# Optimization experiments

Hardware: AMD Instinct MI355X
Metric: run time of the kernel (lower is better)

## Reference

```python
import jax, jax.numpy as jnp
import numpy as np

TOKENS, D_IN = 8192, 1024
E, D_OUT = 8, 1024
H = 2 * D_OUT  # Expert hidden = 2 * num_outputs


def setup_inputs() -> dict:
    key = jax.random.key(0)
    ks = jax.random.split(key, 4)
    s_in = 1.0 / np.sqrt(D_IN)
    s_h = 1.0 / np.sqrt(H)
    return {
        "x": jax.random.normal(ks[0], (TOKENS, D_IN), dtype=jnp.float32),
        "W1": jax.random.normal(ks[1], (E, D_IN, H), dtype=jnp.float32) * s_in,
        "b1": jnp.zeros((E, H), dtype=jnp.float32),
        "W2": jax.random.normal(ks[2], (E, H, D_OUT), dtype=jnp.float32) * s_h,
        "b2": jnp.zeros((E, D_OUT), dtype=jnp.float32),
        "Wg": jax.random.normal(ks[3], (D_IN, E), dtype=jnp.float32) * s_in,
        "bg": jnp.zeros((E,), dtype=jnp.float32),
    }


def reference(x, W1, b1, W2, b2, Wg, bg):
    # Gating: softmax over experts. gates: [N, E]
    gates = jax.nn.softmax(x @ Wg + bg, axis=-1)
    # All experts run densely: batched GEMM over expert axis.
    h = jax.nn.relu(jnp.einsum('nd,edh->neh', x, W1) + b1)       # [N, E, H]
    expert_out = jnp.einsum('neh,ehf->nef', h, W2) + b2          # [N, E, D_OUT]
    # Gate-weighted sum over experts (fused stack*gate->sum).
    return jnp.einsum('nef,ne->nf', expert_out, gates)            # [N, D_OUT]
```

## Files before the change

### kernel.cpp

```cpp
#include <hip/hip_runtime.h>
#include <stdint.h>

#define TOKENS 8192
#define D_IN   1024
#define NEXP   8
#define D_OUT  1024
#define HDIM   2048
#define KBIG   (NEXP * HDIM)

typedef __bf16 bf16x8 __attribute__((ext_vector_type(8)));
typedef __bf16 bf16x4 __attribute__((ext_vector_type(4)));
typedef float  f32x4  __attribute__((ext_vector_type(4)));

__device__ __forceinline__ void gload16(const void* g, void* l) {
  __builtin_amdgcn_global_load_lds(
      (const __attribute__((address_space(1))) void*)g,
      (__attribute__((address_space(3))) void*)l,
      16, 0, 0);
}

__global__ void gate_kernel(const float* __restrict__ x,
                            const float* __restrict__ Wg,
                            const float* __restrict__ bg,
                            float* __restrict__ gates) {
  const int lane = threadIdx.x & 63;
  const int n = blockIdx.x * 4 + (threadIdx.x >> 6);
  float acc[NEXP];
#pragma unroll
  for (int e = 0; e < NEXP; ++e) acc[e] = 0.f;
  const float* xr = x + (size_t)n * D_IN;
  for (int d = lane; d < D_IN; d += 64) {
    float xv = xr[d];
    const float* wr = Wg + d * NEXP;
#pragma unroll
    for (int e = 0; e < NEXP; ++e) acc[e] += xv * wr[e];
  }
#pragma unroll
  for (int e = 0; e < NEXP; ++e) {
    float v = acc[e];
#pragma unroll
    for (int off = 32; off > 0; off >>= 1) v += __shfl_down(v, off);
    acc[e] = v;
  }
  if (lane == 0) {
    float mx = -1e30f;
#pragma unroll
    for (int e = 0; e < NEXP; ++e) { acc[e] += bg[e]; mx = fmaxf(mx, acc[e]); }
    float s = 0.f;
#pragma unroll
    for (int e = 0; e < NEXP; ++e) { acc[e] = expf(acc[e] - mx); s += acc[e]; }
    float inv = 1.f / s;
#pragma unroll
    for (int e = 0; e < NEXP; ++e) gates[n * NEXP + e] = acc[e] * inv;
  }
}

__global__ void cvt_x_kernel(const float* __restrict__ x, __bf16* __restrict__ xb) {
  const int stride = gridDim.x * blockDim.x;
  const int total4 = TOKENS * D_IN / 4;
  for (int i = blockIdx.x * blockDim.x + threadIdx.x; i < total4; i += stride) {
    float4 v = ((const float4*)x)[i];
    bf16x4 o;
    o[0] = (__bf16)v.x; o[1] = (__bf16)v.y; o[2] = (__bf16)v.z; o[3] = (__bf16)v.w;
    ((bf16x4*)xb)[i] = o;
  }
}

__global__ void transpose_cvt_kernel(const float* __restrict__ W,
                                     __bf16* __restrict__ Wt,
                                     int K, int N, int ldo, size_t ebase) {
  __shared__ float tile[32][33];
  const int e = blockIdx.z;
  const float* Win = W + (size_t)e * K * N;
  __bf16* Wout = Wt + (size_t)e * ebase;
  const int n0 = blockIdx.x * 32;
  const int k0 = blockIdx.y * 32;
  const int tx = threadIdx.x & 31;
  const int ty = threadIdx.x >> 5;
#pragma unroll
  for (int r = ty; r < 32; r += 8)
    tile[r][tx] = Win[(size_t)(k0 + r) * N + n0 + tx];
  __syncthreads();
#pragma unroll
  for (int r = ty; r < 32; r += 8)
    Wout[(size_t)(n0 + r) * ldo + k0 + tx] = (__bf16)tile[tx][r];
}

#define BMR 256
#define BNR 128
#define RSLOT ((BMR + BNR) * 64)

template <int EPI>
__global__ __launch_bounds__(512, 1)
void gemm_ring3(const __bf16* __restrict__ A,
                const __bf16* __restrict__ Bbase, size_t Bstride_e,
                const float* __restrict__ biasbase, int bias_stride_e,
                const float* __restrict__ gates,
                const float* __restrict__ b2,
                int e0, int scale_gate, int first,
                __bf16* __restrict__ Hout, float* __restrict__ Fout,
                int M, int N, int K, int ldo, int ocol_stride_e) {
  __shared__ alignas(16) __bf16 lds[3 * RSLOT];

  const int tid  = threadIdx.x;
  const int lane = tid & 63;
  const int wave = tid >> 6;
  const int wr   = wave >> 1;
  const int wc   = wave & 1;
  const int lrow = lane & 15;
  const int khi  = lane >> 4;
  const int e    = e0 + blockIdx.z;

  const __bf16* Bp   = Bbase + (size_t)e * Bstride_e;
  const float*  bias = biasbase + (size_t)e * bias_stride_e;
  const int     ocol0 = e * ocol_stride_e;

  const int Gx   = gridDim.x;
  const int nwg  = Gx * gridDim.y;
  const int orig = blockIdx.y * Gx + blockIdx.x;
  const int wgid = (orig & 7) * (nwg >> 3) + (orig >> 3);
  const int bn0  = (wgid % Gx) * BNR;
  const int bm0  = (wgid / Gx) * BMR;

  const __bf16* gsrc[6];
#pragma unroll
  for (int i = 0; i < 6; ++i) {
    int o    = i * 8192 + tid * 16;
    bool isA = (o < BMR * 128);
    int oo   = isA ? o : (o - BMR * 128);
    int row  = oo >> 7;
    int scb  = (oo & 127) ^ ((row & 7) << 4);
    gsrc[i] = (isA ? A + (size_t)(bm0 + row) * K
                   : Bp + (size_t)(bn0 + row) * K) + (scb >> 1);
  }

  f32x4 acc[4][4];
#pragma unroll
  for (int m = 0; m < 4; ++m)
#pragma unroll
    for (int n = 0; n < 4; ++n) acc[m][n] = f32x4{0.f, 0.f, 0.f, 0.f};

  const int arow0 = wr * 64 + lrow;
  const int brow0 = wc * 64 + lrow;
  const int sx    = (lrow & 7) << 3;

  auto stage2 = [&](int kt, int s, int p) {
    gload16(gsrc[2 * p]     + (size_t)kt * 64, lds + s * RSLOT + (2 * p) * 4096 + wave * 512);
    gload16(gsrc[2 * p + 1] + (size_t)kt * 64, lds + s * RSLOT + (2 * p + 1) * 4096 + wave * 512);
  };

  const int nk = K >> 6;
  stage2(0, 0, 0); stage2(0, 0, 1); stage2(0, 0, 2);
  if (nk > 1) { stage2(1, 1, 0); stage2(1, 1, 1); stage2(1, 1, 2); }

  int s = 0, s2 = 2;
  for (int t = 0; t < nk; ++t) {
    if (t + 1 < nk) asm volatile("s_waitcnt vmcnt(6)" ::: "memory");
    else            asm volatile("s_waitcnt vmcnt(0)" ::: "memory");
    asm volatile("s_barrier" ::: "memory");

    const __bf16* As = lds + s * RSLOT;
    const __bf16* Bs = As + BMR * 64;
    const bool pf = (t + 2 < nk);

    bf16x8 af[4][2], bfv[4][2];
    auto rdA = [&](int m, int kk) {
      af[m][kk] = *(const bf16x8*)&As[(arow0 + m * 16) * 64 + ((kk * 32 + khi * 8) ^ sx)];
    };
    auto rdB = [&](int n, int kk) {
      bfv[n][kk] = *(const bf16x8*)&Bs[(brow0 + n * 16) * 64 + ((kk * 32 + khi * 8) ^ sx)];
    };
    auto mma = [&](int ms, int ns) {
#pragma unroll
      for (int kk = 0; kk < 2; ++kk)
#pragma unroll
        for (int mi = 0; mi < 2; ++mi)
#pragma unroll
          for (int ni = 0; ni < 2; ++ni)
            acc[ms + mi][ns + ni] = __builtin_amdgcn_mfma_f32_16x16x32_bf16(
                af[ms + mi][kk], bfv[ns + ni][kk], acc[ms + mi][ns + ni], 0, 0, 0);
    };

    rdA(0, 0); rdA(0, 1); rdA(1, 0); rdA(1, 1);
    rdB(0, 0); rdB(0, 1); rdB(1, 0); rdB(1, 1);
    if (pf) stage2(t + 2, s2, 0);
    __builtin_amdgcn_sched_barrier(0);
    __builtin_amdgcn_s_setprio(1); mma(0, 0); __builtin_amdgcn_s_setprio(0);
    __builtin_amdgcn_sched_barrier(0);
    rdB(2, 0); rdB(2, 1); rdB(3, 0); rdB(3, 1);
    if (pf) stage2(t + 2, s2, 1);
    __builtin_amdgcn_sched_barrier(0);
    __builtin_amdgcn_s_setprio(1); mma(0, 2); __builtin_amdgcn_s_setprio(0);
    __builtin_amdgcn_sched_barrier(0);
    rdA(2, 0); rdA(2, 1); rdA(3, 0); rdA(3, 1);
    if (pf) stage2(t + 2, s2, 2);
    __builtin_amdgcn_sched_barrier(0);
    __builtin_amdgcn_s_setprio(1); mma(2, 0); __builtin_amdgcn_s_setprio(0);
    __builtin_amdgcn_sched_barrier(0);
    __builtin_amdgcn_s_setprio(1); mma(2, 2); __builtin_amdgcn_s_setprio(0);

    s  = (s == 2) ? 0 : s + 1;
    s2 = (s2 == 2) ? 0 : s2 + 1;
  }

#pragma unroll
  for (int m = 0; m < 4; ++m) {
    const int grow0 = bm0 + wr * 64 + m * 16 + khi * 4;
    if constexpr (EPI == 0) {
      float g[4];
      if (scale_gate) {
#pragma unroll
        for (int r = 0; r < 4; ++r) g[r] = gates[(size_t)(grow0 + r) * NEXP + e];
      } else {
#pragma unroll
        for (int r = 0; r < 4; ++r) g[r] = 1.f;
      }
#pragma unroll
      for (int n = 0; n < 4; ++n) {
        const int lc = bn0 + wc * 64 + n * 16 + lrow;
        const float bv = bias[lc];
        f32x4 a = acc[m][n];
#pragma unroll
        for (int r = 0; r < 4; ++r) {
          float v = a[r] + bv;
          v = v > 0.f ? v : 0.f;
          Hout[(size_t)(grow0 + r) * ldo + ocol0 + lc] = (__bf16)(v * g[r]);
        }
      }
    } else if constexpr (EPI == 1) {
      float g[4];
#pragma unroll
      for (int r = 0; r < 4; ++r) g[r] = gates[(size_t)(grow0 + r) * NEXP + e];
#pragma unroll
      for (int n = 0; n < 4; ++n) {
        const int lc = bn0 + wc * 64 + n * 16 + lrow;
        const float bv = bias[lc];
        f32x4 a = acc[m][n];
#pragma unroll
        for (int r = 0; r < 4; ++r) {
          float v = (a[r] + bv) * g[r];
          float* o = Fout + (size_t)(grow0 + r) * ldo + lc;
          if (first) *o = v;
          else       *o += v;
        }
      }
    } else {
      float gv[4][NEXP];
#pragma unroll
      for (int r = 0; r < 4; ++r)
#pragma unroll
        for (int j = 0; j < NEXP; ++j)
          gv[r][j] = gates[(size_t)(grow0 + r) * NEXP + j];
#pragma unroll
      for (int n = 0; n < 4; ++n) {
        const int lc = bn0 + wc * 64 + n * 16 + lrow;
        float b2v[NEXP];
#pragma unroll
        for (int j = 0; j < NEXP; ++j) b2v[j] = b2[j * N + lc];
        f32x4 a = acc[m][n];
#pragma unroll
        for (int r = 0; r < 4; ++r) {
          float bias2 = 0.f;
#pragma unroll
          for (int j = 0; j < NEXP; ++j) bias2 += gv[r][j] * b2v[j];
          Fout[(size_t)(grow0 + r) * ldo + lc] = a[r] + bias2;
        }
      }
    }
  }
}

extern "C" void kernel_launch(void* const* d_in, const int* in_sizes, int n_in,
                              void* d_out, int out_size, void* d_ws, size_t ws_size,
                              hipStream_t stream) {
  const float* x  = (const float*)d_in[0];
  const float* W1 = (const float*)d_in[1];
  const float* b1 = (const float*)d_in[2];
  const float* W2 = (const float*)d_in[3];
  const float* b2 = (const float*)d_in[4];
  const float* Wg = (const float*)d_in[5];
  const float* bg = (const float*)d_in[6];
  float* out = (float*)d_out;

  char* w = (char*)d_ws;
  float* gates = (float*)w;   w += (size_t)TOKENS * NEXP * 4;
  __bf16* xb   = (__bf16*)w;  w += (size_t)TOKENS * D_IN * 2;
  __bf16* w1t  = (__bf16*)w;  w += (size_t)NEXP * HDIM * D_IN * 2;
  __bf16* w2t  = (__bf16*)w;  w += (size_t)NEXP * D_OUT * HDIM * 2;
  __bf16* hbuf = (__bf16*)w;

  const size_t need_fused =
      (size_t)TOKENS * NEXP * 4 + (size_t)TOKENS * D_IN * 2 +
      (size_t)NEXP * HDIM * D_IN * 2 + (size_t)NEXP * D_OUT * HDIM * 2 +
      (size_t)TOKENS * KBIG * 2;
  const bool fused = (ws_size >= need_fused);

  gate_kernel<<<TOKENS / 4, 256, 0, stream>>>(x, Wg, bg, gates);
  cvt_x_kernel<<<2048, 256, 0, stream>>>(x, xb);
  transpose_cvt_kernel<<<dim3(HDIM / 32, D_IN / 32, NEXP), 256, 0, stream>>>(
      W1, w1t, D_IN, HDIM, D_IN, (size_t)HDIM * D_IN);

  if (fused) {
    transpose_cvt_kernel<<<dim3(D_OUT / 32, HDIM / 32, NEXP), 256, 0, stream>>>(
        W2, w2t, HDIM, D_OUT, KBIG, (size_t)HDIM);
    gemm_ring3<0><<<dim3(HDIM / BNR, TOKENS / BMR, NEXP), 512, 0, stream>>>(
        xb, w1t, (size_t)HDIM * D_IN, b1, HDIM, gates, nullptr,
        0, 1, 0, hbuf, nullptr, TOKENS, HDIM, D_IN, KBIG, HDIM);
    gemm_ring3<2><<<dim3(D_OUT / BNR, TOKENS / BMR, 1), 512, 0, stream>>>(
        hbuf, w2t, 0, b2, 0, gates, b2,
        0, 0, 0, nullptr, out, TOKENS, D_OUT, KBIG, D_OUT, 0);
  } else {
    transpose_cvt_kernel<<<dim3(D_OUT / 32, HDIM / 32, NEXP), 256, 0, stream>>>(
        W2, w2t, HDIM, D_OUT, HDIM, (size_t)D_OUT * HDIM);
    for (int e = 0; e < NEXP; ++e) {
      gemm_ring3<0><<<dim3(HDIM / BNR, TOKENS / BMR, 1), 512, 0, stream>>>(
          xb, w1t, (size_t)HDIM * D_IN, b1, HDIM, gates, nullptr,
          e, 0, 0, hbuf, nullptr, TOKENS, HDIM, D_IN, HDIM, 0);
      gemm_ring3<1><<<dim3(D_OUT / BNR, TOKENS / BMR, 1), 512, 0, stream>>>(
          hbuf, w2t, (size_t)D_OUT * HDIM, b2, D_OUT, gates, nullptr,
          e, 0, (e == 0) ? 1 : 0, nullptr, out, TOKENS, D_OUT, HDIM, D_OUT, 0);
    }
  }
}
```

Measured before the change: 760.7 us.

## Replace 3-stage GEMM ring with templated 4-stage K=32 pipeline and larger tiles

Rewrites the bf16 MFMA GEMM as a templated kernel with a 4-slot LDS ring over K-steps of 32 and a prefetch distance of three. Block and warp tiles become template parameters: the first GEMM uses 256x256 tiles over a 2x4 wave grid, and the second keeps 256x128. The XOR swizzle on LDS is dropped, and the MFMA work is split into sub-steps with barriers between them. The aim is more load/compute overlap and more reuse per tile in the first GEMM. In exchange it adds more barriers per K-step, and the unswizzled LDS reads risk bank conflicts.

```diff
diff --git a/kernel.cpp b/kernel.cpp
--- a/kernel.cpp
+++ b/kernel.cpp
@@ -86,27 +86,29 @@
     Wout[(size_t)(n0 + r) * ldo + k0 + tx] = (__bf16)tile[tx][r];
 }
 
-#define BMR 256
-#define BNR 128
-#define RSLOT ((BMR + BNR) * 64)
-
-template <int EPI>
-__global__ __launch_bounds__(512, 1)
-void gemm_ring3(const __bf16* __restrict__ A,
-                const __bf16* __restrict__ Bbase, size_t Bstride_e,
-                const float* __restrict__ biasbase, int bias_stride_e,
-                const float* __restrict__ gates,
-                const float* __restrict__ b2,
-                int e0, int scale_gate, int first,
-                __bf16* __restrict__ Hout, float* __restrict__ Fout,
-                int M, int N, int K, int ldo, int ocol_stride_e) {
-  __shared__ alignas(16) __bf16 lds[3 * RSLOT];
+template <int BM, int BN, int WM, int WN, int NSUB, int EPI>
+__global__ __launch_bounds__(512, 2)
+void gemm_pipe(const __bf16* __restrict__ A,
+               const __bf16* __restrict__ Bbase, size_t Bstride_e,
+               const float* __restrict__ biasbase, int bias_stride_e,
+               const float* __restrict__ gates,
+               const float* __restrict__ b2,
+               int e0, int scale_gate, int first,
+               __bf16* __restrict__ Hout, float* __restrict__ Fout,
+               int M, int N, int K, int ldo, int ocol_stride_e) {
+  constexpr int RM = BM / WM, RN = BN / WN;
+  constexpr int FM = RM / 16, FN = RN / 16;
+  constexpr int GM = FM / NSUB;
+  constexpr int SLOT  = (BM + BN) * 32;
+  constexpr int LOADS = (BM + BN) * 64 / 8192;
+  constexpr int LPS   = LOADS / NSUB;
+  __shared__ alignas(16) __bf16 lds[4 * SLOT];
 
   const int tid  = threadIdx.x;
   const int lane = tid & 63;
   const int wave = tid >> 6;
-  const int wr   = wave >> 1;
-  const int wc   = wave & 1;
+  const int wr   = wave / WN;
+  const int wc   = wave % WN;
   const int lrow = lane & 15;
   const int khi  = lane >> 4;
   const int e    = e0 + blockIdx.z;
@@ -119,93 +121,93 @@
   const int nwg  = Gx * gridDim.y;
   const int orig = blockIdx.y * Gx + blockIdx.x;
   const int wgid = (orig & 7) * (nwg >> 3) + (orig >> 3);
-  const int bn0  = (wgid % Gx) * BNR;
-  const int bm0  = (wgid / Gx) * BMR;
-
-  const __bf16* gsrc[6];
-#pragma unroll
-  for (int i = 0; i < 6; ++i) {
+  const int bn0  = (wgid % Gx) * BN;
+  const int bm0  = (wgid / Gx) * BM;
+
+  const __bf16* gsrc[LOADS];
+#pragma unroll
+  for (int i = 0; i < LOADS; ++i) {
     int o    = i * 8192 + tid * 16;
-    bool isA = (o < BMR * 128);
-    int oo   = isA ? o : (o - BMR * 128);
-    int row  = oo >> 7;
-    int scb  = (oo & 127) ^ ((row & 7) << 4);
+    bool isA = (o < BM * 64);
+    int oo   = isA ? o : (o - BM * 64);
+    int row  = oo >> 6;
+    int cb   = oo & 63;
     gsrc[i] = (isA ? A + (size_t)(bm0 + row) * K
-                   : Bp + (size_t)(bn0 + row) * K) + (scb >> 1);
-  }
-
-  f32x4 acc[4][4];
-#pragma unroll
-  for (int m = 0; m < 4; ++m)
-#pragma unroll
-    for (int n = 0; n < 4; ++n) acc[m][n] = f32x4{0.f, 0.f, 0.f, 0.f};
-
-  const int arow0 = wr * 64 + lrow;
-  const int brow0 = wc * 64 + lrow;
-  const int sx    = (lrow & 7) << 3;
-
-  auto stage2 = [&](int kt, int s, int p) {
-    gload16(gsrc[2 * p]     + (size_t)kt * 64, lds + s * RSLOT + (2 * p) * 4096 + wave * 512);
-    gload16(gsrc[2 * p + 1] + (size_t)kt * 64, lds + s * RSLOT + (2 * p + 1) * 4096 + wave * 512);
-  };
-
-  const int nk = K >> 6;
-  stage2(0, 0, 0); stage2(0, 0, 1); stage2(0, 0, 2);
-  if (nk > 1) { stage2(1, 1, 0); stage2(1, 1, 1); stage2(1, 1, 2); }
-
-  int s = 0, s2 = 2;
+                   : Bp + (size_t)(bn0 + row) * K) + (cb >> 1);
+  }
+
+  f32x4 acc[FM][FN];
+#pragma unroll
+  for (int m = 0; m < FM; ++m)
+#pragma unroll
+    for (int n = 0; n < FN; ++n) acc[m][n] = f32x4{0.f, 0.f, 0.f, 0.f};
+
+  const int nk = K >> 5;
+
+#pragma unroll
+  for (int pt = 0; pt < 3; ++pt)
+#pragma unroll
+    for (int i = 0; i < LOADS; ++i)
+      gload16(gsrc[i] + (size_t)pt * 32, lds + pt * SLOT + i * 4096 + wave * 512);
+  if constexpr (LOADS == 4) asm volatile("s_waitcnt vmcnt(8)" ::: "memory");
+  else                      asm volatile("s_waitcnt vmcnt(6)" ::: "memory");
+  asm volatile("s_barrier" ::: "memory");
+
   for (int t = 0; t < nk; ++t) {
-    if (t + 1 < nk) asm volatile("s_waitcnt vmcnt(6)" ::: "memory");
-    else            asm volatile("s_waitcnt vmcnt(0)" ::: "memory");
-    asm volatile("s_barrier" ::: "memory");
-
-    const __bf16* As = lds + s * RSLOT;
-    const __bf16* Bs = As + BMR * 64;
-    const bool pf = (t + 2 < nk);
-
-    bf16x8 af[4][2], bfv[4][2];
-    auto rdA = [&](int m, int kk) {
-      af[m][kk] = *(const bf16x8*)&As[(arow0 + m * 16) * 64 + ((kk * 32 + khi * 8) ^ sx)];
-    };
-    auto rdB = [&](int n, int kk) {
-      bfv[n][kk] = *(const bf16x8*)&Bs[(brow0 + n * 16) * 64 + ((kk * 32 + khi * 8) ^ sx)];
-    };
-    auto mma = [&](int ms, int ns) {
-#pragma unroll
-      for (int kk = 0; kk < 2; ++kk)
-#pragma unroll
-        for (int mi = 0; mi < 2; ++mi)
-#pragma unroll
-          for (int ni = 0; ni < 2; ++ni)
-            acc[ms + mi][ns + ni] = __builtin_amdgcn_mfma_f32_16x16x32_bf16(
-                af[ms + mi][kk], bfv[ns + ni][kk], acc[ms + mi][ns + ni], 0, 0, 0);
-    };
-
-    rdA(0, 0); rdA(0, 1); rdA(1, 0); rdA(1, 1);
-    rdB(0, 0); rdB(0, 1); rdB(1, 0); rdB(1, 1);
-    if (pf) stage2(t + 2, s2, 0);
-    __builtin_amdgcn_sched_barrier(0);
-    __builtin_amdgcn_s_setprio(1); mma(0, 0); __builtin_amdgcn_s_setprio(0);
-    __builtin_amdgcn_sched_barrier(0);
-    rdB(2, 0); rdB(2, 1); rdB(3, 0); rdB(3, 1);
-    if (pf) stage2(t + 2, s2, 1);
-    __builtin_amdgcn_sched_barrier(0);
-    __builtin_amdgcn_s_setprio(1); mma(0, 2); __builtin_amdgcn_s_setprio(0);
-    __builtin_amdgcn_sched_barrier(0);
-    rdA(2, 0); rdA(2, 1); rdA(3, 0); rdA(3, 1);
-    if (pf) stage2(t + 2, s2, 2);
-    __builtin_amdgcn_sched_barrier(0);
-    __builtin_amdgcn_s_setprio(1); mma(2, 0); __builtin_amdgcn_s_setprio(0);
-    __builtin_amdgcn_sched_barrier(0);
-    __builtin_amdgcn_s_setprio(1); mma(2, 2); __builtin_amdgcn_s_setprio(0);
-
-    s  = (s == 2) ? 0 : s + 1;
-    s2 = (s2 == 2) ? 0 : s2 + 1;
-  }
-
-#pragma unroll
-  for (int m = 0; m < 4; ++m) {
-    const int grow0 = bm0 + wr * 64 + m * 16 + khi * 4;
+    const __bf16* As = lds + (t & 3) * SLOT;
+    const __bf16* Bs = As + BM * 32;
+    __bf16* ldst = lds + ((t + 3) & 3) * SLOT;
+    const bool pf = (t + 3 < nk);
+    bf16x8 bfr[FN];
+
+#pragma unroll
+    for (int q = 0; q < NSUB; ++q) {
+      bf16x8 af[GM];
+      if (q == 0) {
+#pragma unroll
+        for (int n = 0; n < FN; ++n)
+          bfr[n] = *(const bf16x8*)&Bs[(wc * RN + n * 16 + lrow) * 32 + khi * 8];
+      }
+#pragma unroll
+      for (int mi = 0; mi < GM; ++mi)
+        af[mi] = *(const bf16x8*)&As[(wr * RM + (q * GM + mi) * 16 + lrow) * 32 + khi * 8];
+      if (pf) {
+#pragma unroll
+        for (int j = 0; j < LPS; ++j) {
+          const int i = q * LPS + j;
+          gload16(gsrc[i] + (size_t)(t + 3) * 32, ldst + i * 4096 + wave * 512);
+        }
+      }
+      asm volatile("s_barrier" ::: "memory");
+      asm volatile("s_waitcnt lgkmcnt(0)" ::: "memory");
+      __builtin_amdgcn_sched_barrier(0);
+      __builtin_amdgcn_s_setprio(1);
+#pragma unroll
+      for (int mi = 0; mi < GM; ++mi)
+#pragma unroll
+        for (int n = 0; n < FN; ++n)
+          acc[q * GM + mi][n] = __builtin_amdgcn_mfma_f32_16x16x32_bf16(
+              af[mi], bfr[n], acc[q * GM + mi][n], 0, 0, 0);
+      __builtin_amdgcn_s_setprio(0);
+      __builtin_amdgcn_sched_barrier(0);
+      if (q == NSUB - 1 && t < nk - 1) {
+        if (t + 3 <= nk - 1) {
+          if constexpr (LOADS == 4) asm volatile("s_waitcnt vmcnt(8)" ::: "memory");
+          else                      asm volatile("s_waitcnt vmcnt(6)" ::: "memory");
+        } else if (t + 2 <= nk - 1) {
+          if constexpr (LOADS == 4) asm volatile("s_waitcnt vmcnt(4)" ::: "memory");
+          else                      asm volatile("s_waitcnt vmcnt(3)" ::: "memory");
+        } else {
+          asm volatile("s_waitcnt vmcnt(0)" ::: "memory");
+        }
+      }
+      asm volatile("s_barrier" ::: "memory");
+    }
+  }
+
+#pragma unroll
+  for (int m = 0; m < FM; ++m) {
+    const int grow0 = bm0 + wr * RM + m * 16 + khi * 4;
     if constexpr (EPI == 0) {
       float g[4];
       if (scale_gate) {
@@ -216,8 +218,8 @@
         for (int r = 0; r < 4; ++r) g[r] = 1.f;
       }
 #pragma unroll
-      for (int n = 0; n < 4; ++n) {
-        const int lc = bn0 + wc * 64 + n * 16 + lrow;
+      for (int n = 0; n < FN; ++n) {
+        const int lc = bn0 + wc * RN + n * 16 + lrow;
         const float bv = bias[lc];
         f32x4 a = acc[m][n];
 #pragma unroll
@@ -232,8 +234,8 @@
 #pragma unroll
       for (int r = 0; r < 4; ++r) g[r] = gates[(size_t)(grow0 + r) * NEXP + e];
 #pragma unroll
-      for (int n = 0; n < 4; ++n) {
-        const int lc = bn0 + wc * 64 + n * 16 + lrow;
+      for (int n = 0; n < FN; ++n) {
+        const int lc = bn0 + wc * RN + n * 16 + lrow;
         const float bv = bias[lc];
         f32x4 a = acc[m][n];
 #pragma unroll
@@ -252,8 +254,8 @@
         for (int j = 0; j < NEXP; ++j)
           gv[r][j] = gates[(size_t)(grow0 + r) * NEXP + j];
 #pragma unroll
-      for (int n = 0; n < 4; ++n) {
-        const int lc = bn0 + wc * 64 + n * 16 + lrow;
+      for (int n = 0; n < FN; ++n) {
+        const int lc = bn0 + wc * RN + n * 16 + lrow;
         float b2v[NEXP];
 #pragma unroll
         for (int j = 0; j < NEXP; ++j) b2v[j] = b2[j * N + lc];
@@ -303,20 +305,20 @@
   if (fused) {
     transpose_cvt_kernel<<<dim3(D_OUT / 32, HDIM / 32, NEXP), 256, 0, stream>>>(
         W2, w2t, HDIM, D_OUT, KBIG, (size_t)HDIM);
-    gemm_ring3<0><<<dim3(HDIM / BNR, TOKENS / BMR, NEXP), 512, 0, stream>>>(
+    gemm_pipe<256, 256, 2, 4, 2, 0><<<dim3(HDIM / 256, TOKENS / 256, NEXP), 512, 0, stream>>>(
         xb, w1t, (size_t)HDIM * D_IN, b1, HDIM, gates, nullptr,
         0, 1, 0, hbuf, nullptr, TOKENS, HDIM, D_IN, KBIG, HDIM);
-    gemm_ring3<2><<<dim3(D_OUT / BNR, TOKENS / BMR, 1), 512, 0, stream>>>(
+    gemm_pipe<256, 128, 4, 2, 1, 2><<<dim3(D_OUT / 128, TOKENS / 256, 1), 512, 0, stream>>>(
         hbuf, w2t, 0, b2, 0, gates, b2,
         0, 0, 0, nullptr, out, TOKENS, D_OUT, KBIG, D_OUT, 0);
   } else {
     transpose_cvt_kernel<<<dim3(D_OUT / 32, HDIM / 32, NEXP), 256, 0, stream>>>(
         W2, w2t, HDIM, D_OUT, HDIM, (size_t)D_OUT * HDIM);
     for (int e = 0; e < NEXP; ++e) {
-      gemm_ring3<0><<<dim3(HDIM / BNR, TOKENS / BMR, 1), 512, 0, stream>>>(
+      gemm_pipe<256, 256, 2, 4, 2, 0><<<dim3(HDIM / 256, TOKENS / 256, 1), 512, 0, stream>>>(
           xb, w1t, (size_t)HDIM * D_IN, b1, HDIM, gates, nullptr,
           e, 0, 0, hbuf, nullptr, TOKENS, HDIM, D_IN, HDIM, 0);
-      gemm_ring3<1><<<dim3(D_OUT / BNR, TOKENS / BMR, 1), 512, 0, stream>>>(
+      gemm_pipe<256, 128, 4, 2, 1, 1><<<dim3(D_OUT / 128, TOKENS / 256, 1), 512, 0, stream>>>(
           hbuf, w2t, (size_t)D_OUT * HDIM, b2, D_OUT, gates, nullptr,
           e, 0, (e == 0) ? 1 : 0, nullptr, out, TOKENS, D_OUT, HDIM, D_OUT, 0);
     }
```

New measurement: 882.6 us. 1.16x slower.
